# Performance work log

Hardware: AMD Instinct MI355X
Metric: run time of the kernel (lower is better)

The kernel has to match this reference:

```python
import jax, jax.numpy as jnp
import numpy as np

B, L, D = 1, 4096, 1024
H = 16
HD = D // H
SCALE = HD ** -0.5


def setup_inputs() -> dict:
    key = jax.random.key(0)
    k1, k2, k3 = jax.random.split(key, 3)
    X = jax.random.normal(k1, (B, L, D), dtype=jnp.float32)
    # torch Linear default init ~ U(-1/sqrt(fan_in), 1/sqrt(fan_in)); scaled normals are fine for a reference
    Wqkv = jax.random.normal(k2, (D, 3 * D), dtype=jnp.float32) * (D ** -0.5)
    bqkv = jnp.zeros((3 * D,), dtype=jnp.float32)
    Wproj = jax.random.normal(k3, (D, D), dtype=jnp.float32) * (D ** -0.5)
    bproj = jnp.zeros((D,), dtype=jnp.float32)
    return {"X": X, "Wqkv": Wqkv, "bqkv": bqkv, "Wproj": Wproj, "bproj": bproj}


def reference(X, Wqkv, bqkv, Wproj, bproj):
    Bn, Ln, Dn = X.shape
    qkv = X @ Wqkv + bqkv                       # [B, L, 3D]
    qkv = qkv.reshape(Bn, Ln, 3, H, HD)
    q, k, v = qkv[:, :, 0], qkv[:, :, 1], qkv[:, :, 2]   # [B, L, H, HD]
    # attention scores [B, H, L, L] (naive, matches original)
    attn = jnp.einsum('bqhd,bkhd->bhqk', q, k) * SCALE
    causal = jnp.tril(jnp.ones((Ln, Ln), dtype=bool))     # True = keep
    attn = jnp.where(causal, attn, -jnp.inf)
    score = jax.nn.softmax(attn, axis=-1)
    out = jnp.einsum('bhqk,bkhd->bqhd', score, v)         # [B, L, H, HD]
    out = out.reshape(Bn, Ln, Dn)
    return out @ Wproj + bproj
```

## Files before the change

kernel.cpp:

```cpp
#include <hip/hip_runtime.h>
#include <hip/hip_bf16.h>
#include <string.h>


typedef unsigned short ushort_t;
typedef __attribute__((ext_vector_type(8))) short short8;
typedef __attribute__((ext_vector_type(4))) float f32x4;

#define MFMA16(a, b, c) __builtin_amdgcn_mfma_f32_16x16x32_bf16(a, b, c, 0, 0, 0)

static constexpr int Lq = 4096;
static constexpr int Dm = 1024;
static constexpr int NH = 16;
static constexpr int HD = 64;
static constexpr int D3 = 3072;
static constexpr float SCALE_LOG2E = 0.125f * 1.44269504088896340736f;

__device__ __forceinline__ ushort_t f2bf(float f) {
    union { float f; unsigned int u; } x{f};
    unsigned int u = x.u;
    u += 0x7fffu + ((u >> 16) & 1u);
    return (ushort_t)(u >> 16);
}

__device__ __forceinline__ unsigned int cvtpk(float a, float b) {
    __hip_bfloat162 h = __float22bfloat162_rn(make_float2(a, b));
    unsigned int u;
    memcpy(&u, &h, 4);
    return u;
}

__device__ __forceinline__ void gl2lds16(const ushort_t* g, ushort_t* l) {
    __builtin_amdgcn_global_load_lds(
        (const __attribute__((address_space(1))) unsigned int*)g,
        (__attribute__((address_space(3))) unsigned int*)l, 16, 0, 0);
}

__global__ void cvt_bf16(const float* __restrict__ in, ushort_t* __restrict__ out, int n) {
    int i = (blockIdx.x * blockDim.x + threadIdx.x) * 4;
    if (i + 3 < n) {
        float4 v = *(const float4*)&in[i];
        ushort_t r[4] = { f2bf(v.x), f2bf(v.y), f2bf(v.z), f2bf(v.w) };
        *(uint2*)&out[i] = *(uint2*)r;
    }
}

__global__ void wtrans(const float* __restrict__ W, ushort_t* __restrict__ Wt, int K, int N) {
    __shared__ float tile[32][33];
    int nb = blockIdx.x * 32, kb = blockIdx.y * 32;
    int tx = threadIdx.x, ty = threadIdx.y;
    for (int j = 0; j < 32; j += 8)
        tile[ty + j][tx] = W[(size_t)(kb + ty + j) * N + nb + tx];
    __syncthreads();
    for (int j = 0; j < 32; j += 8)
        Wt[(size_t)(nb + ty + j) * K + kb + tx] = f2bf(tile[tx][ty + j]);
}

__global__ void vtrans(const ushort_t* __restrict__ qkv, ushort_t* __restrict__ Vt) {
    __shared__ ushort_t tile[32][33];
    int h  = blockIdx.z;
    int lb = blockIdx.x * 32;
    int db = blockIdx.y * 32;
    int tx = threadIdx.x, ty = threadIdx.y;
    for (int j = 0; j < 32; j += 8)
        tile[ty + j][tx] = qkv[(size_t)(lb + ty + j) * D3 + 2048 + h * HD + db + tx];
    __syncthreads();
    const int key  = lb + tx;
    const int k63  = key & 63;
    const int cp   = (key & ~63) + ((k63 & 15) * 4 + (k63 >> 4));
    for (int j = 0; j < 32; j += 8)
        Vt[(size_t)h * HD * Lq + (size_t)(db + ty + j) * Lq + cp] = tile[tx][ty + j];
}

template <bool OUT_BF16, bool QSCALE>
__global__ void __launch_bounds__(256)
gemm_bt(const ushort_t* __restrict__ A, const ushort_t* __restrict__ Bt,
        const float* __restrict__ bias, void* __restrict__ C,
        int M, int N, int K) {
    __shared__ alignas(16) ushort_t Alds[128 * 32];
    __shared__ alignas(16) ushort_t Blds[128 * 32];
    const int tid  = threadIdx.x;
    const int lane = tid & 63;
    const int w    = tid >> 6;
    const int quad = lane >> 4;
    const int l16  = lane & 15;
    const int mbase = blockIdx.x * 128;
    const int nbase = blockIdx.y * 128;
    const int moff  = (w >> 1) * 64;
    const int noff  = (w & 1) * 64;

    f32x4 acc[4][4] = {};

    for (int kb = 0; kb < K; kb += 32) {
        __syncthreads();
        #pragma unroll
        for (int c = 0; c < 2; c++) {
            int id  = w * 128 + c * 64 + lane;
            int row = id >> 2, col = (id & 3) * 8;
            gl2lds16(&A[(size_t)(mbase + row) * K + kb + col], &Alds[(size_t)(w * 128 + c * 64) * 8]);
            gl2lds16(&Bt[(size_t)(nbase + row) * K + kb + col], &Blds[(size_t)(w * 128 + c * 64) * 8]);
        }
        __syncthreads();
        short8 a[4], b[4];
        #pragma unroll
        for (int m = 0; m < 4; m++)
            a[m] = *(const short8*)&Alds[(moff + m * 16 + l16) * 32 + quad * 8];
        #pragma unroll
        for (int n = 0; n < 4; n++)
            b[n] = *(const short8*)&Blds[(noff + n * 16 + l16) * 32 + quad * 8];
        #pragma unroll
        for (int m = 0; m < 4; m++)
            #pragma unroll
            for (int n = 0; n < 4; n++)
                acc[m][n] = MFMA16(a[m], b[n], acc[m][n]);
    }

    #pragma unroll
    for (int m = 0; m < 4; m++)
        #pragma unroll
        for (int n = 0; n < 4; n++)
            #pragma unroll
            for (int r = 0; r < 4; r++) {
                int row = mbase + moff + m * 16 + quad * 4 + r;
                int col = nbase + noff + n * 16 + l16;
                float v = acc[m][n][r] + bias[col];
                if (QSCALE && col < Dm) v *= SCALE_LOG2E;
                if (OUT_BF16)
                    ((ushort_t*)C)[(size_t)row * N + col] = f2bf(v);
                else
                    ((float*)C)[(size_t)row * N + col] = v;
            }
}

__global__ void __launch_bounds__(512, 2)
attn_fwd(const ushort_t* __restrict__ qkv, const ushort_t* __restrict__ Vt,
         ushort_t* __restrict__ O) {
    __shared__ alignas(16) ushort_t Kl[2][2][64 * 64];
    __shared__ alignas(16) ushort_t Vl[2][2][64 * 64];
    __shared__ alignas(16) ushort_t Pl[8 * 32 * 72];
    __shared__ alignas(16) float    Ml[256 * 41];

    const int tid  = threadIdx.x;
    const int lane = tid & 63;
    const int w    = tid >> 6;
    const int half = w >> 2;
    const int sub  = w & 3;
    const int quad = lane >> 4;
    const int l16  = lane & 15;
    const int bid  = blockIdx.x;
    const int h    = bid & 15;
    const int p    = bid >> 4;
    ushort_t* pw   = Pl + w * 32 * 72;
    const float NEG_INF = -__builtin_inff();
    const int sw   = l16 & 7;

    const short bf1 = (short)0x3F80;
    const short8 ones = { bf1, bf1, bf1, bf1, bf1, bf1, bf1, bf1 };

    const ushort_t* kbase = qkv + Dm + h * HD;
    const ushort_t* vbase = Vt + (size_t)h * HD * Lq;

    int kvo[4][2];
    #pragma unroll
    for (int s = 0; s < 4; s++)
        #pragma unroll
        for (int kh = 0; kh < 2; kh++)
            kvo[s][kh] = (s * 16 + l16) * 64 + (((kh * 4 + quad) ^ sw) * 8);

    const int rr = tid >> 3, cc = (tid & 7) ^ (rr & 7);
    const ushort_t* kse = kbase + (size_t)rr * D3 + cc * 8;
    const ushort_t* vse = vbase + (size_t)rr * Lq + cc * 8;
    const int dstoff = w * 512;

    for (int sel = 0; sel < 2; sel++) {
        const int c      = sel ? (31 - p) : p;
        const int qc     = c * 128;
        const int rounds = c + 1;
        const int qw     = qc + sub * 32;

        short8 qf[2][2];
        #pragma unroll
        for (int m = 0; m < 2; m++) {
            const ushort_t* qr = qkv + (size_t)(qw + m * 16 + l16) * D3 + h * HD;
            qf[m][0] = *(const short8*)(qr + quad * 8);
            qf[m][1] = *(const short8*)(qr + 32 + quad * 8);
        }

        f32x4 o[2][4] = {};
        f32x4 lacc[2] = {};

        const ushort_t* kp = kse;
        const ushort_t* vp = vse;

        auto stage = [&](int b) {
            gl2lds16(kp,            &Kl[0][b][dstoff]);
            gl2lds16(kp + 64 * D3,  &Kl[1][b][dstoff]);
            gl2lds16(vp,            &Vl[0][b][dstoff]);
            gl2lds16(vp + 64,       &Vl[1][b][dstoff]);
            kp += (size_t)128 * D3;
            vp += 128;
        };

        stage(0);

        for (int r = 0; r < rounds; r++) {
            const int buf = r & 1;
            __syncthreads();
            if (r + 1 < rounds) stage(buf ^ 1);

            const ushort_t* Kb = &Kl[half][buf][0];
            const ushort_t* Vb = &Vl[half][buf][0];
            const int k0 = (2 * r + half) * 64;
            const bool domask = (r == rounds - 1);

            short8 kf[4][2];
            #pragma unroll
            for (int s = 0; s < 4; s++)
                #pragma unroll
                for (int kh = 0; kh < 2; kh++)
                    kf[s][kh] = *(const short8*)&Kb[kvo[s][kh]];

            f32x4 st[2][4];
            #pragma unroll
            for (int m = 0; m < 2; m++)
                #pragma unroll
                for (int s = 0; s < 4; s++) {
                    f32x4 t = {};
                    t = MFMA16(qf[m][0], kf[s][0], t);
                    t = MFMA16(qf[m][1], kf[s][1], t);
                    st[m][s] = t;
                }

            #pragma unroll
            for (int m = 0; m < 2; m++)
                #pragma unroll
                for (int r4 = 0; r4 < 4; r4++) {
                    float e[4];
                    #pragma unroll
                    for (int s = 0; s < 4; s++) {
                        float v = st[m][s][r4];
                        if (domask) {
                            const int qg = qw + m * 16 + quad * 4 + r4;
                            if (k0 + s * 16 + l16 > qg) v = NEG_INF;
                        }
                        e[s] = __builtin_amdgcn_exp2f(v);
                    }
                    uint2 pk = { cvtpk(e[0], e[1]), cvtpk(e[2], e[3]) };
                    *(uint2*)&pw[(m * 16 + quad * 4 + r4) * 72 + l16 * 4] = pk;
                }

            short8 pf[2][2];
            #pragma unroll
            for (int m = 0; m < 2; m++)
                #pragma unroll
                for (int kh = 0; kh < 2; kh++)
                    pf[m][kh] = *(const short8*)&pw[(m * 16 + l16) * 72 + kh * 32 + quad * 8];
            #pragma unroll
            for (int m = 0; m < 2; m++) {
                lacc[m] = MFMA16(pf[m][0], ones, lacc[m]);
                lacc[m] = MFMA16(pf[m][1], ones, lacc[m]);
            }

            short8 vf[4][2];
            #pragma unroll
            for (int t = 0; t < 4; t++)
                #pragma unroll
                for (int kh = 0; kh < 2; kh++)
                    vf[t][kh] = *(const short8*)&Vb[kvo[t][kh]];
            #pragma unroll
            for (int m = 0; m < 2; m++)
                #pragma unroll
                for (int t = 0; t < 4; t++) {
                    o[m][t] = MFMA16(pf[m][0], vf[t][0], o[m][t]);
                    o[m][t] = MFMA16(pf[m][1], vf[t][1], o[m][t]);
                }
        }

        __syncthreads();
        if (half == 1) {
            float* dst = Ml + (sub * 64 + lane) * 41;
            #pragma unroll
            for (int m = 0; m < 2; m++)
                #pragma unroll
                for (int t = 0; t < 4; t++)
                    *(f32x4*)(dst + m * 16 + t * 4) = o[m][t];
            *(f32x4*)(dst + 32) = lacc[0];
            *(f32x4*)(dst + 36) = lacc[1];
        }
        __syncthreads();
        if (half == 0) {
            const float* src = Ml + (sub * 64 + lane) * 41;
            #pragma unroll
            for (int m = 0; m < 2; m++)
                #pragma unroll
                for (int t = 0; t < 4; t++)
                    o[m][t] += *(const f32x4*)(src + m * 16 + t * 4);
            lacc[0] += *(const f32x4*)(src + 32);
            lacc[1] += *(const f32x4*)(src + 36);
            #pragma unroll
            for (int m = 0; m < 2; m++)
                #pragma unroll
                for (int r4 = 0; r4 < 4; r4++) {
                    const float inv = 1.0f / lacc[m][r4];
                    ushort_t* orow = O + (size_t)(qw + m * 16 + quad * 4 + r4) * Dm + h * HD;
                    #pragma unroll
                    for (int t = 0; t < 4; t++)
                        orow[t * 16 + l16] = f2bf(o[m][t][r4] * inv);
                }
        }
        __syncthreads();
    }
}

extern "C" void kernel_launch(void* const* d_in, const int* in_sizes, int n_in,
                              void* d_out, int out_size, void* d_ws, size_t ws_size,
                              hipStream_t stream) {
    const float* X     = (const float*)d_in[0];
    const float* Wqkv  = (const float*)d_in[1];
    const float* bqkv  = (const float*)d_in[2];
    const float* Wproj = (const float*)d_in[3];
    const float* bproj = (const float*)d_in[4];
    float* out = (float*)d_out;

    ushort_t* ws     = (ushort_t*)d_ws;
    ushort_t* Xb     = ws;
    ushort_t* WqkvT  = Xb + (size_t)Lq * Dm;
    ushort_t* WprojT = WqkvT + (size_t)D3 * Dm;
    ushort_t* qkvB   = WprojT + (size_t)Dm * Dm;
    ushort_t* VtB    = qkvB + (size_t)Lq * D3;
    ushort_t* Ob     = VtB + (size_t)NH * HD * Lq;

    cvt_bf16<<<(Lq * Dm / 4 + 255) / 256, 256, 0, stream>>>(X, Xb, Lq * Dm);
    wtrans<<<dim3(D3 / 32, Dm / 32), dim3(32, 8), 0, stream>>>(Wqkv, WqkvT, Dm, D3);
    wtrans<<<dim3(Dm / 32, Dm / 32), dim3(32, 8), 0, stream>>>(Wproj, WprojT, Dm, Dm);

    gemm_bt<true, true><<<dim3(Lq / 128, D3 / 128), 256, 0, stream>>>(
        Xb, WqkvT, bqkv, (void*)qkvB, Lq, D3, Dm);

    vtrans<<<dim3(Lq / 32, HD / 32, NH), dim3(32, 8), 0, stream>>>(qkvB, VtB);

    attn_fwd<<<dim3(256), 512, 0, stream>>>(qkvB, VtB, Ob);

    gemm_bt<false, false><<<dim3(Lq / 128, Dm / 128), 256, 0, stream>>>(
        Ob, WprojT, bproj, (void*)out, Lq, Dm, Dm);
}
```

Measured before the change: 222.5 us.

## Fuse prep kernels, write V transposed from QKV GEMM epilogue, retile proj GEMM

```diff
diff --git a/kernel.cpp b/kernel.cpp
--- a/kernel.cpp
+++ b/kernel.cpp
@@ -36,47 +36,39 @@
         (__attribute__((address_space(3))) unsigned int*)l, 16, 0, 0);
 }
 
-__global__ void cvt_bf16(const float* __restrict__ in, ushort_t* __restrict__ out, int n) {
-    int i = (blockIdx.x * blockDim.x + threadIdx.x) * 4;
-    if (i + 3 < n) {
-        float4 v = *(const float4*)&in[i];
+__global__ void __launch_bounds__(256)
+prep(const float* __restrict__ X, const float* __restrict__ Wqkv,
+     const float* __restrict__ Wproj, ushort_t* __restrict__ Xb,
+     ushort_t* __restrict__ WqkvT, ushort_t* __restrict__ WprojT) {
+    __shared__ float tile[32][33];
+    const int bid = blockIdx.x, tid = threadIdx.x;
+    if (bid < 4096) {
+        int i = (bid * 256 + tid) * 4;
+        float4 v = *(const float4*)&X[i];
         ushort_t r[4] = { f2bf(v.x), f2bf(v.y), f2bf(v.z), f2bf(v.w) };
-        *(uint2*)&out[i] = *(uint2*)r;
-    }
-}
-
-__global__ void wtrans(const float* __restrict__ W, ushort_t* __restrict__ Wt, int K, int N) {
-    __shared__ float tile[32][33];
-    int nb = blockIdx.x * 32, kb = blockIdx.y * 32;
-    int tx = threadIdx.x, ty = threadIdx.y;
+        *(uint2*)&Xb[i] = *(uint2*)r;
+        return;
+    }
+    const float* W; ushort_t* Wt; int Nd, nb, kb;
+    if (bid < 7168) {
+        int b = bid - 4096; W = Wqkv;  Wt = WqkvT;  Nd = 3072;
+        nb = (b % 96) * 32; kb = (b / 96) * 32;
+    } else {
+        int b = bid - 7168; W = Wproj; Wt = WprojT; Nd = 1024;
+        nb = (b % 32) * 32; kb = (b / 32) * 32;
+    }
+    const int tx = tid & 31, ty = tid >> 5;
     for (int j = 0; j < 32; j += 8)
-        tile[ty + j][tx] = W[(size_t)(kb + ty + j) * N + nb + tx];
+        tile[ty + j][tx] = W[(size_t)(kb + ty + j) * Nd + nb + tx];
     __syncthreads();
     for (int j = 0; j < 32; j += 8)
-        Wt[(size_t)(nb + ty + j) * K + kb + tx] = f2bf(tile[tx][ty + j]);
-}
-
-__global__ void vtrans(const ushort_t* __restrict__ qkv, ushort_t* __restrict__ Vt) {
-    __shared__ ushort_t tile[32][33];
-    int h  = blockIdx.z;
-    int lb = blockIdx.x * 32;
-    int db = blockIdx.y * 32;
-    int tx = threadIdx.x, ty = threadIdx.y;
-    for (int j = 0; j < 32; j += 8)
-        tile[ty + j][tx] = qkv[(size_t)(lb + ty + j) * D3 + 2048 + h * HD + db + tx];
-    __syncthreads();
-    const int key  = lb + tx;
-    const int k63  = key & 63;
-    const int cp   = (key & ~63) + ((k63 & 15) * 4 + (k63 >> 4));
-    for (int j = 0; j < 32; j += 8)
-        Vt[(size_t)h * HD * Lq + (size_t)(db + ty + j) * Lq + cp] = tile[tx][ty + j];
-}
-
-template <bool OUT_BF16, bool QSCALE>
+        Wt[(size_t)(nb + ty + j) * Dm + kb + tx] = f2bf(tile[tx][ty + j]);
+}
+
 __global__ void __launch_bounds__(256)
-gemm_bt(const ushort_t* __restrict__ A, const ushort_t* __restrict__ Bt,
-        const float* __restrict__ bias, void* __restrict__ C,
-        int M, int N, int K) {
+gemm_qkv(const ushort_t* __restrict__ A, const ushort_t* __restrict__ Bt,
+         const float* __restrict__ bias, ushort_t* __restrict__ Cq,
+         ushort_t* __restrict__ Vt) {
     __shared__ alignas(16) ushort_t Alds[128 * 32];
     __shared__ alignas(16) ushort_t Blds[128 * 32];
     const int tid  = threadIdx.x;
@@ -88,6 +80,7 @@
     const int nbase = blockIdx.y * 128;
     const int moff  = (w >> 1) * 64;
     const int noff  = (w & 1) * 64;
+    const int K = Dm;
 
     f32x4 acc[4][4] = {};
 
@@ -115,21 +108,35 @@
                 acc[m][n] = MFMA16(a[m], b[n], acc[m][n]);
     }
 
-    #pragma unroll
-    for (int m = 0; m < 4; m++)
-        #pragma unroll
-        for (int n = 0; n < 4; n++)
+    if (nbase < 2048) {
+        const bool qscale = (nbase < 1024);
+        #pragma unroll
+        for (int m = 0; m < 4; m++)
+            #pragma unroll
+            for (int n = 0; n < 4; n++)
+                #pragma unroll
+                for (int r = 0; r < 4; r++) {
+                    int row = mbase + moff + m * 16 + quad * 4 + r;
+                    int col = nbase + noff + n * 16 + l16;
+                    float v = acc[m][n][r] + bias[col];
+                    if (qscale) v *= SCALE_LOG2E;
+                    Cq[(size_t)row * D3 + col] = f2bf(v);
+                }
+    } else {
+        #pragma unroll
+        for (int m = 0; m < 4; m++)
             #pragma unroll
             for (int r = 0; r < 4; r++) {
-                int row = mbase + moff + m * 16 + quad * 4 + r;
-                int col = nbase + noff + n * 16 + l16;
-                float v = acc[m][n][r] + bias[col];
-                if (QSCALE && col < Dm) v *= SCALE_LOG2E;
-                if (OUT_BF16)
-                    ((ushort_t*)C)[(size_t)row * N + col] = f2bf(v);
-                else
-                    ((float*)C)[(size_t)row * N + col] = v;
+                const int key = mbase + moff + m * 16 + quad * 4 + r;
+                const int cp  = (key & ~63) + ((key & 15) * 4 + ((key >> 4) & 3));
+                #pragma unroll
+                for (int n = 0; n < 4; n++) {
+                    const int col = nbase + noff + n * 16 + l16;
+                    float v = acc[m][n][r] + bias[col];
+                    Vt[(size_t)(col - 2048) * Lq + cp] = f2bf(v);
+                }
             }
+    }
 }
 
 __global__ void __launch_bounds__(512, 2)
@@ -193,10 +200,10 @@
         const ushort_t* vp = vse;
 
         auto stage = [&](int b) {
-            gl2lds16(kp,            &Kl[0][b][dstoff]);
-            gl2lds16(kp + 64 * D3,  &Kl[1][b][dstoff]);
-            gl2lds16(vp,            &Vl[0][b][dstoff]);
-            gl2lds16(vp + 64,       &Vl[1][b][dstoff]);
+            gl2lds16(kp,           &Kl[0][b][dstoff]);
+            gl2lds16(kp + 64 * D3, &Kl[1][b][dstoff]);
+            gl2lds16(vp,           &Vl[0][b][dstoff]);
+            gl2lds16(vp + 64,      &Vl[1][b][dstoff]);
             kp += (size_t)128 * D3;
             vp += 128;
         };
@@ -312,6 +319,64 @@
     }
 }
 
+__global__ void __launch_bounds__(256)
+gemm_proj(const ushort_t* __restrict__ A, const ushort_t* __restrict__ Bt,
+          const float* __restrict__ bias, float* __restrict__ C) {
+    __shared__ alignas(16) ushort_t Alds[128 * 32];
+    __shared__ alignas(16) ushort_t Blds[64 * 32];
+    const int tid  = threadIdx.x;
+    const int lane = tid & 63;
+    const int w    = tid >> 6;
+    const int quad = lane >> 4;
+    const int l16  = lane & 15;
+    const int mbase = blockIdx.x * 128;
+    const int nbase = blockIdx.y * 64;
+    const int moff  = (w >> 1) * 64;
+    const int noff  = (w & 1) * 32;
+    const int K = Dm, N = Dm;
+
+    f32x4 acc[4][2] = {};
+
+    for (int kb = 0; kb < K; kb += 32) {
+        __syncthreads();
+        #pragma unroll
+        for (int c = 0; c < 2; c++) {
+            int id  = w * 128 + c * 64 + lane;
+            int row = id >> 2, col = (id & 3) * 8;
+            gl2lds16(&A[(size_t)(mbase + row) * K + kb + col], &Alds[(size_t)(w * 128 + c * 64) * 8]);
+        }
+        {
+            int id  = w * 64 + lane;
+            int row = id >> 2, col = (id & 3) * 8;
+            gl2lds16(&Bt[(size_t)(nbase + row) * K + kb + col], &Blds[(size_t)(w * 64) * 8]);
+        }
+        __syncthreads();
+        short8 a[4], b[2];
+        #pragma unroll
+        for (int m = 0; m < 4; m++)
+            a[m] = *(const short8*)&Alds[(moff + m * 16 + l16) * 32 + quad * 8];
+        #pragma unroll
+        for (int n = 0; n < 2; n++)
+            b[n] = *(const short8*)&Blds[(noff + n * 16 + l16) * 32 + quad * 8];
+        #pragma unroll
+        for (int m = 0; m < 4; m++)
+            #pragma unroll
+            for (int n = 0; n < 2; n++)
+                acc[m][n] = MFMA16(a[m], b[n], acc[m][n]);
+    }
+
+    #pragma unroll
+    for (int m = 0; m < 4; m++)
+        #pragma unroll
+        for (int n = 0; n < 2; n++)
+            #pragma unroll
+            for (int r = 0; r < 4; r++) {
+                int row = mbase + moff + m * 16 + quad * 4 + r;
+                int col = nbase + noff + n * 16 + l16;
+                C[(size_t)row * N + col] = acc[m][n][r] + bias[col];
+            }
+}
+
 extern "C" void kernel_launch(void* const* d_in, const int* in_sizes, int n_in,
                               void* d_out, int out_size, void* d_ws, size_t ws_size,
                               hipStream_t stream) {
@@ -330,17 +395,13 @@
     ushort_t* VtB    = qkvB + (size_t)Lq * D3;
     ushort_t* Ob     = VtB + (size_t)NH * HD * Lq;
 
-    cvt_bf16<<<(Lq * Dm / 4 + 255) / 256, 256, 0, stream>>>(X, Xb, Lq * Dm);
-    wtrans<<<dim3(D3 / 32, Dm / 32), dim3(32, 8), 0, stream>>>(Wqkv, WqkvT, Dm, D3);
-    wtrans<<<dim3(Dm / 32, Dm / 32), dim3(32, 8), 0, stream>>>(Wproj, WprojT, Dm, Dm);
-
-    gemm_bt<true, true><<<dim3(Lq / 128, D3 / 128), 256, 0, stream>>>(
-        Xb, WqkvT, bqkv, (void*)qkvB, Lq, D3, Dm);
-
-    vtrans<<<dim3(Lq / 32, HD / 32, NH), dim3(32, 8), 0, stream>>>(qkvB, VtB);
+    prep<<<dim3(8192), 256, 0, stream>>>(X, Wqkv, Wproj, Xb, WqkvT, WprojT);
+
+    gemm_qkv<<<dim3(Lq / 128, D3 / 128), 256, 0, stream>>>(
+        Xb, WqkvT, bqkv, qkvB, VtB);
 
     attn_fwd<<<dim3(256), 512, 0, stream>>>(qkvB, VtB, Ob);
 
-    gemm_bt<false, false><<<dim3(Lq / 128, Dm / 128), 256, 0, stream>>>(
-        Ob, WprojT, bproj, (void*)out, Lq, Dm, Dm);
-}
+    gemm_proj<<<dim3(Lq / 128, Dm / 64), 256, 0, stream>>>(
+        Ob, WprojT, bproj, out);
+}
```

New measurement: 214.4 us. 3.7% less time.
